# Performance work log

Hardware: AMD Instinct MI355X
Metric: run time of the kernel (lower is better)

The kernel has to match this reference:

```python
import math
import jax, jax.numpy as jnp
import numpy as np

B, N, E, H, DPOS = 64, 196, 768, 16, 3
DH = E // H


def rel_pos(num_patches):
    # deterministic relative-position encodings [N, N, 3] = (dx, dy, d^2)
    v = int(math.isqrt(num_patches))
    ind = jnp.arange(v)[None, :] - jnp.arange(v)[:, None]          # [v, v]
    indx = jnp.tile(ind, (v, v))                                    # [N, N]
    indy = jnp.repeat(jnp.repeat(ind, v, axis=0), v, axis=1)       # [N, N]
    indd = indx ** 2 + indy ** 2
    return jnp.stack([indx, indy, indd], axis=-1).astype(jnp.float32)


def setup_inputs() -> dict:
    key = jax.random.key(0)
    ks = jax.random.split(key, 9)
    std = 0.02  # trunc_normal std used by the module's init
    return {
        "q": jax.random.normal(ks[0], (B, N, E), jnp.float32),
        "k": jax.random.normal(ks[1], (B, N, E), jnp.float32),
        "v": jax.random.normal(ks[2], (B, N, E), jnp.float32),
        "mask": jnp.ones((B, 1, N, N), jnp.bool_),
        "Wq": jax.random.normal(ks[3], (E, E), jnp.float32) * std,
        "Wk": jax.random.normal(ks[4], (E, E), jnp.float32) * std,
        "Wv": jax.random.normal(ks[5], (E, E), jnp.float32) * std,
        "Wo": jax.random.normal(ks[6], (E, E), jnp.float32) * std,
        "bo": jnp.zeros((E,), jnp.float32),
        "Wpos": jax.random.normal(ks[7], (H, DPOS), jnp.float32) * std,
        "bpos": jnp.zeros((H,), jnp.float32),
        "gating": jnp.ones((H,), jnp.float32),
    }


def reference(q, k, v, mask, Wq, Wk, Wv, Wo, bo, Wpos, bpos, gating):
    b, n, _ = q.shape

    def heads(x, W):  # [b, n, E] -> [b, H, n, DH]
        return (x @ W.T).reshape(b, n, H, DH).transpose(0, 2, 1, 3)

    Q, K, V = heads(q, Wq), heads(k, Wk), heads(v, Wv)

    energy = jnp.einsum('bhqd,bhkd->bhqk', Q, K) / math.sqrt(DH)
    energy = jnp.where(mask, energy, -jnp.inf)
    content = jax.nn.softmax(energy, axis=-1)                      # [b, H, n, n]

    rel = rel_pos(n)                                               # [n, n, 3]
    pos = jnp.einsum('qkp,hp->hqk', rel, Wpos) + bpos[:, None, None]
    pos = jax.nn.softmax(pos, axis=-1)[None]                       # [1, H, n, n]

    g = jax.nn.sigmoid(gating)[None, :, None, None]
    score = (1.0 - g) * content + g * pos
    score = score / jnp.sum(score, axis=-1, keepdims=True)

    attn = jnp.einsum('bhqk,bhkd->bhqd', score, V)
    out = attn.transpose(0, 2, 1, 3).reshape(b, n, E) @ Wo.T + bo
    return out
```

## Files before the change

kernel.cpp:

```cpp
#include <hip/hip_runtime.h>
#include <hip/hip_bf16.h>

#define BB 64
#define NN 196
#define EE 768
#define HH 16
#define DHH 48

typedef short bf16x8 __attribute__((ext_vector_type(8)));
typedef float f32x4 __attribute__((ext_vector_type(4)));
typedef unsigned short u16;
typedef unsigned short u16x8 __attribute__((ext_vector_type(8)));
typedef unsigned int u32;

static __device__ __forceinline__ u16 f2bf(float f) {
  union { float f; u32 u; } un; un.f = f;
  u32 u = un.u;
  u32 r = (u + 0x7fffu + ((u >> 16) & 1u)) >> 16;
  return (u16)r;
}

static __device__ __forceinline__ u16 f2bf_hw(float f) {
  __hip_bfloat16 h = __float2bfloat16(f);
  return __builtin_bit_cast(u16, h);
}

#define GLOAD16(GP, LP)                                                        \
  __builtin_amdgcn_global_load_lds(                                            \
      (const __attribute__((address_space(1))) void*)(GP),                     \
      (__attribute__((address_space(3))) void*)(LP), 16, 0, 0)

static __device__ __forceinline__ int xcd_swz(int bid, int nwg) {
  int q = nwg >> 3, r = nwg & 7;
  int xcd = bid & 7, i = bid >> 3;
  return (xcd < r ? xcd * (q + 1) : r * (q + 1) + (xcd - r) * q) + i;
}

__global__ __launch_bounds__(64) void pos_kernel(const float* __restrict__ Wpos,
                                                 const float* __restrict__ bpos,
                                                 float* __restrict__ pos) {
  int bid = blockIdx.x;
  int h = bid / NN, q = bid % NN;
  int lane = threadIdx.x;
  float w0 = Wpos[h * 3 + 0], w1 = Wpos[h * 3 + 1], w2 = Wpos[h * 3 + 2];
  float bb = bpos[h];
  int qx = q % 14, qy = q / 14;
  float e[4];
  float mx = -1e30f;
#pragma unroll
  for (int i = 0; i < 4; ++i) {
    int k = lane + 64 * i;
    float val = -1e30f;
    if (k < NN) {
      int kx = k % 14, ky = k / 14;
      float dx = (float)(kx - qx), dy = (float)(ky - qy);
      val = w0 * dx + w1 * dy + w2 * (dx * dx + dy * dy) + bb;
    }
    e[i] = val;
    mx = fmaxf(mx, val);
  }
#pragma unroll
  for (int off = 1; off < 64; off <<= 1) mx = fmaxf(mx, __shfl_xor(mx, off));
  float s = 0.f;
#pragma unroll
  for (int i = 0; i < 4; ++i) {
    int k = lane + 64 * i;
    float p = (k < NN) ? expf(e[i] - mx) : 0.f;
    e[i] = p;
    s += p;
  }
#pragma unroll
  for (int off = 1; off < 64; off <<= 1) s += __shfl_xor(s, off);
  float inv = 1.f / s;
#pragma unroll
  for (int i = 0; i < 4; ++i) {
    int k = lane + 64 * i;
    if (k < NN) pos[(size_t)h * NN * NN + (size_t)q * NN + k] = e[i] * inv;
  }
}

__global__ __launch_bounds__(256) void cvtw_kernel(const float* __restrict__ W0,
                                                   const float* __restrict__ W1,
                                                   const float* __restrict__ W2,
                                                   const float* __restrict__ W3,
                                                   u16* __restrict__ out) {
  const float* Ws[4] = {W0, W1, W2, W3};
  int mat = blockIdx.y;
  const float* src = Ws[mat];
  int idx = blockIdx.x * 256 + threadIdx.x;
  float4 f = ((const float4*)src)[idx];
  short4 s;
  s.x = (short)f2bf_hw(f.x);
  s.y = (short)f2bf_hw(f.y);
  s.z = (short)f2bf_hw(f.z);
  s.w = (short)f2bf_hw(f.w);
  *(short4*)(out + (size_t)mat * EE * EE + (size_t)idx * 4) = s;
}

template <bool A_F32, bool OUT_F32>
static __device__ __forceinline__ void gemm_body(const void* __restrict__ Aptr,
                                                 const u16* __restrict__ Wb,
                                                 void* __restrict__ Yptr,
                                                 const float* __restrict__ bias,
                                                 int m0, int n0) {
  constexpr int ABYTES = A_F32 ? (128 * 32 * 4) : (128 * 32 * 2);
  __shared__ unsigned char Asb[2][ABYTES];
  __shared__ u16 Bs[2][128 * 32];
  const int tid = threadIdx.x;
  const int lane = tid & 63, wid = tid >> 6;
  const int wm = wid >> 1, wn = wid & 1;
  const int r16 = lane & 15, g4 = lane >> 4;
  f32x4 acc[4][4];
#pragma unroll
  for (int i = 0; i < 4; ++i)
#pragma unroll
    for (int j = 0; j < 4; ++j) acc[i][j] = (f32x4){0.f, 0.f, 0.f, 0.f};

  auto stage = [&](int buf, int k0) {
#pragma unroll
    for (int c = 0; c < 2; ++c) {
      int s = c * 256 + tid;
      GLOAD16(Wb + (size_t)(n0 + (s >> 2)) * EE + k0 + (s & 3) * 8,
              (u16*)&Bs[buf][0] + s * 8);
    }
    if (A_F32) {
#pragma unroll
      for (int c = 0; c < 4; ++c) {
        int s = c * 256 + tid;
        int row = s >> 3;
        int cf = ((s & 7) ^ (row & 7)) * 4;
        GLOAD16((const float*)Aptr + (size_t)(m0 + row) * EE + k0 + cf,
                &Asb[buf][0] + s * 16);
      }
    } else {
#pragma unroll
      for (int c = 0; c < 2; ++c) {
        int s = c * 256 + tid;
        GLOAD16((const u16*)Aptr + (size_t)(m0 + (s >> 2)) * EE + k0 + (s & 3) * 8,
                &Asb[buf][0] + s * 16);
      }
    }
  };

  stage(0, 0);
  __syncthreads();
  int buf = 0;
  for (int t = 0; t < 24; ++t) {
    if (t < 23) stage(buf ^ 1, (t + 1) * 32);
    bf16x8 af[4], bfr[4];
#pragma unroll
    for (int i = 0; i < 4; ++i) {
      int r = wm * 64 + i * 16 + r16;
      if (A_F32) {
        const char* rowp = (const char*)&Asb[buf][0] + r * 128;
        int lo = (g4 * 32) ^ ((r & 7) << 4);
        f32x4 l4 = *(const f32x4*)(rowp + lo);
        f32x4 h4 = *(const f32x4*)(rowp + (lo ^ 16));
        u16x8 fr;
        fr[0] = f2bf_hw(l4[0]); fr[1] = f2bf_hw(l4[1]);
        fr[2] = f2bf_hw(l4[2]); fr[3] = f2bf_hw(l4[3]);
        fr[4] = f2bf_hw(h4[0]); fr[5] = f2bf_hw(h4[1]);
        fr[6] = f2bf_hw(h4[2]); fr[7] = f2bf_hw(h4[3]);
        af[i] = __builtin_bit_cast(bf16x8, fr);
      } else {
        af[i] = *(const bf16x8*)((const u16*)&Asb[buf][0] + r * 32 + g4 * 8);
      }
    }
#pragma unroll
    for (int j = 0; j < 4; ++j)
      bfr[j] = *(const bf16x8*)&Bs[buf][(wn * 64 + j * 16 + r16) * 32 + g4 * 8];
#pragma unroll
    for (int i = 0; i < 4; ++i)
#pragma unroll
      for (int j = 0; j < 4; ++j)
        acc[i][j] = __builtin_amdgcn_mfma_f32_16x16x32_bf16(af[i], bfr[j], acc[i][j], 0, 0, 0);
    __syncthreads();
    buf ^= 1;
  }
#pragma unroll
  for (int i = 0; i < 4; ++i) {
    int row = m0 + wm * 64 + i * 16 + g4 * 4;
#pragma unroll
    for (int j = 0; j < 4; ++j) {
      int col = n0 + wn * 64 + j * 16 + r16;
#pragma unroll
      for (int v = 0; v < 4; ++v) {
        float val = acc[i][j][v];
        if (OUT_F32)
          ((float*)Yptr)[(size_t)(row + v) * EE + col] = val + bias[col];
        else
          ((u16*)Yptr)[(size_t)(row + v) * EE + col] = f2bf(val);
      }
    }
  }
}

__global__ __launch_bounds__(256) void qkv_gemm(const float* __restrict__ q,
                                                const float* __restrict__ k,
                                                const float* __restrict__ v,
                                                const u16* __restrict__ Wqb,
                                                const u16* __restrict__ Wkb,
                                                const u16* __restrict__ Wvb,
                                                u16* __restrict__ Qp,
                                                u16* __restrict__ Kp,
                                                u16* __restrict__ Vp) {
  int sid = xcd_swz(blockIdx.x, 3 * 98 * 6);
  int z = sid / 588, rem = sid % 588;
  int m0 = (rem / 6) * 128, n0 = (rem % 6) * 128;
  const float* A = (z == 0) ? q : (z == 1) ? k : v;
  const u16* W = (z == 0) ? Wqb : (z == 1) ? Wkb : Wvb;
  u16* Y = (z == 0) ? Qp : (z == 1) ? Kp : Vp;
  gemm_body<true, false>(A, W, Y, nullptr, m0, n0);
}

__global__ __launch_bounds__(256) void out_gemm(const u16* __restrict__ ctx,
                                                const u16* __restrict__ Wob,
                                                float* __restrict__ out,
                                                const float* __restrict__ bo) {
  int sid = xcd_swz(blockIdx.x, 98 * 6);
  int m0 = (sid / 6) * 128, n0 = (sid % 6) * 128;
  gemm_body<false, true>(ctx, Wob, out, bo, m0, n0);
}

__global__ __launch_bounds__(512) void attn_kernel(const u16* __restrict__ Qp,
                                                   const u16* __restrict__ Kp,
                                                   const u16* __restrict__ Vp,
                                                   const float* __restrict__ pos,
                                                   const float* __restrict__ gating,
                                                   u16* __restrict__ ctx) {
  __shared__ u16 Qs[208 * 72];
  __shared__ u16 Ks[208 * 72];
  __shared__ u16 Vt[48 * 232];
  __shared__ u16 sc[8][16 * 232];
  int bh = blockIdx.x;
  int b = bh >> 4, h = bh & 15;
  int tid = threadIdx.x;
  {
    u32* z = (u32*)&Qs[0];
    for (int i = tid; i < (208 * 72) / 2; i += 512) z[i] = 0u;
    z = (u32*)&Ks[0];
    for (int i = tid; i < (208 * 72) / 2; i += 512) z[i] = 0u;
    z = (u32*)&Vt[0];
    for (int i = tid; i < (48 * 232) / 2; i += 512) z[i] = 0u;
  }
  __syncthreads();
  const u16* Qb = Qp + (size_t)b * NN * EE + h * DHH;
  const u16* Kb = Kp + (size_t)b * NN * EE + h * DHH;
  const u16* Vb = Vp + (size_t)b * NN * EE + h * DHH;
  for (int c = tid; c < NN * 12; c += 512) {
    int row = c / 12, k4 = (c % 12) * 4;
    short4 v = *(const short4*)(Qb + (size_t)row * EE + k4);
    *(short4*)&Qs[row * 72 + k4] = v;
  }
  for (int c = tid; c < NN * 12; c += 512) {
    int row = c / 12, k4 = (c % 12) * 4;
    short4 v = *(const short4*)(Kb + (size_t)row * EE + k4);
    *(short4*)&Ks[row * 72 + k4] = v;
  }
  for (int c = tid; c < NN * 12; c += 512) {
    int key = c / 12, d4 = (c % 12) * 4;
    short4 v = *(const short4*)(Vb + (size_t)key * EE + d4);
    Vt[(d4 + 0) * 232 + key] = (u16)v.x;
    Vt[(d4 + 1) * 232 + key] = (u16)v.y;
    Vt[(d4 + 2) * 232 + key] = (u16)v.z;
    Vt[(d4 + 3) * 232 + key] = (u16)v.w;
  }
  __syncthreads();

  int wid = tid >> 6, lane = tid & 63;
  int r16 = lane & 15, g4 = lane >> 4;
  float g = 1.f / (1.f + expf(-gating[h]));
  float omg = 1.f - g;
  u16* scw = &sc[wid][0];
  const float scale = 0.14433756729740643f;
  const float* posh = pos + (size_t)h * NN * NN;

  for (int rt = wid; rt < 13; rt += 8) {
    int q0 = rt * 16;
    bf16x8 aQ0 = *(const bf16x8*)&Qs[(q0 + r16) * 72 + g4 * 8];
    bf16x8 aQ1 = *(const bf16x8*)&Qs[(q0 + r16) * 72 + 32 + g4 * 8];
    f32x4 e[13];
#pragma unroll
    for (int ct = 0; ct < 13; ++ct) {
      bf16x8 b0 = *(const bf16x8*)&Ks[(ct * 16 + r16) * 72 + g4 * 8];
      bf16x8 b1 = *(const bf16x8*)&Ks[(ct * 16 + r16) * 72 + 32 + g4 * 8];
      f32x4 t = (f32x4){0.f, 0.f, 0.f, 0.f};
      t = __builtin_amdgcn_mfma_f32_16x16x32_bf16(aQ0, b0, t, 0, 0, 0);
      t = __builtin_amdgcn_mfma_f32_16x16x32_bf16(aQ1, b1, t, 0, 0, 0);
      e[ct] = t;
    }
    float mx[4] = {-1e30f, -1e30f, -1e30f, -1e30f};
#pragma unroll
    for (int ct = 0; ct < 13; ++ct) {
      int cix = ct * 16 + r16;
      bool valid = cix < NN;
#pragma unroll
      for (int v = 0; v < 4; ++v) {
        float ev = e[ct][v] * scale;
        ev = valid ? ev : -1e30f;
        e[ct][v] = ev;
        mx[v] = fmaxf(mx[v], ev);
      }
    }
#pragma unroll
    for (int v = 0; v < 4; ++v)
#pragma unroll
      for (int off = 1; off < 16; off <<= 1) mx[v] = fmaxf(mx[v], __shfl_xor(mx[v], off));
    float sm[4] = {0.f, 0.f, 0.f, 0.f};
#pragma unroll
    for (int ct = 0; ct < 13; ++ct)
#pragma unroll
      for (int v = 0; v < 4; ++v) {
        float p = __expf(e[ct][v] - mx[v]);
        e[ct][v] = p;
        sm[v] += p;
      }
#pragma unroll
    for (int v = 0; v < 4; ++v)
#pragma unroll
      for (int off = 1; off < 16; off <<= 1) sm[v] += __shfl_xor(sm[v], off);
    float inv[4];
#pragma unroll
    for (int v = 0; v < 4; ++v) inv[v] = 1.f / sm[v];
    int qg[4];
#pragma unroll
    for (int v = 0; v < 4; ++v) qg[v] = q0 + g4 * 4 + v;
    float t2[4] = {0.f, 0.f, 0.f, 0.f};
#pragma unroll
    for (int ct = 0; ct < 13; ++ct) {
      int cix = ct * 16 + r16;
      bool valid = cix < NN;
#pragma unroll
      for (int v = 0; v < 4; ++v) {
        float content = e[ct][v] * inv[v];
        float pv = 0.f;
        if (valid && qg[v] < NN) pv = posh[(size_t)qg[v] * NN + cix];
        float s = omg * content + g * pv;
        e[ct][v] = s;
        t2[v] += s;
      }
    }
#pragma unroll
    for (int v = 0; v < 4; ++v)
#pragma unroll
      for (int off = 1; off < 16; off <<= 1) t2[v] += __shfl_xor(t2[v], off);
    float inv2[4];
#pragma unroll
    for (int v = 0; v < 4; ++v) inv2[v] = 1.f / t2[v];
#pragma unroll
    for (int ct = 0; ct < 14; ++ct)
#pragma unroll
      for (int v = 0; v < 4; ++v) {
        float s = (ct < 13) ? e[ct][v] * inv2[v] : 0.f;
        scw[(g4 * 4 + v) * 232 + ct * 16 + r16] = f2bf(s);
      }
    asm volatile("s_waitcnt lgkmcnt(0)" ::: "memory");
#pragma unroll
    for (int dt = 0; dt < 3; ++dt) {
      f32x4 pv = (f32x4){0.f, 0.f, 0.f, 0.f};
#pragma unroll
      for (int kt = 0; kt < 7; ++kt) {
        bf16x8 aS = *(const bf16x8*)&scw[r16 * 232 + kt * 32 + g4 * 8];
        bf16x8 bV = *(const bf16x8*)&Vt[(dt * 16 + r16) * 232 + kt * 32 + g4 * 8];
        pv = __builtin_amdgcn_mfma_f32_16x16x32_bf16(aS, bV, pv, 0, 0, 0);
      }
#pragma unroll
      for (int v = 0; v < 4; ++v) {
        if (qg[v] < NN)
          ctx[((size_t)b * NN + qg[v]) * EE + h * DHH + dt * 16 + r16] = f2bf(pv[v]);
      }
    }
  }
}

extern "C" void kernel_launch(void* const* d_in, const int* in_sizes, int n_in,
                              void* d_out, int out_size, void* d_ws, size_t ws_size,
                              hipStream_t stream) {
  const float* q = (const float*)d_in[0];
  const float* k = (const float*)d_in[1];
  const float* v = (const float*)d_in[2];
  const float* Wq = (const float*)d_in[4];
  const float* Wk = (const float*)d_in[5];
  const float* Wv = (const float*)d_in[6];
  const float* Wo = (const float*)d_in[7];
  const float* bo = (const float*)d_in[8];
  const float* Wpos = (const float*)d_in[9];
  const float* bpos = (const float*)d_in[10];
  const float* gating = (const float*)d_in[11];
  float* out = (float*)d_out;

  char* ws = (char*)d_ws;
  const size_t elems = (size_t)BB * NN * EE;
  u16* Qp = (u16*)ws;
  u16* Kp = Qp + elems;
  u16* Vp = Kp + elems;
  u16* ctx = Vp + elems;
  float* pos = (float*)(ws + 4 * elems * sizeof(u16));
  u16* Wqb = (u16*)(ws + 4 * elems * sizeof(u16) + (size_t)HH * NN * NN * sizeof(float));
  u16* Wkb = Wqb + (size_t)EE * EE;
  u16* Wvb = Wkb + (size_t)EE * EE;
  u16* Wob = Wvb + (size_t)EE * EE;

  hipLaunchKernelGGL(pos_kernel, dim3(HH * NN), dim3(64), 0, stream, Wpos, bpos, pos);
  hipLaunchKernelGGL(cvtw_kernel, dim3(EE * EE / 4 / 256, 4), dim3(256), 0, stream,
                     Wq, Wk, Wv, Wo, Wqb);

  hipLaunchKernelGGL(qkv_gemm, dim3(3 * 98 * 6), dim3(256), 0, stream,
                     q, k, v, Wqb, Wkb, Wvb, Qp, Kp, Vp);

  hipLaunchKernelGGL(attn_kernel, dim3(BB * HH), dim3(512), 0, stream,
                     Qp, Kp, Vp, pos, gating, ctx);

  hipLaunchKernelGGL(out_gemm, dim3(98 * 6), dim3(256), 0, stream,
                     ctx, Wob, out, bo);
}
```

Baseline: 200.5 us.

## Widen GEMM tiles to 128x256 and convert fp32 A to bf16 once per stage

The QKV and output GEMMs now use 128x256 tiles, so each wave computes 64x128 and the block count halves (882 and 294 blocks). The fp32 activation tile is now loaded into registers, converted to bf16 once and written to shared memory after the MFMA loop. Before, fp32 was staged in LDS and converted on every fragment read. This cuts LDS footprint and repeated conversion work and reuses A across more columns, but doubles accumulator registers (launch bounds 256,2) and gives fewer blocks to fill the CUs.

```diff
diff --git a/kernel.cpp b/kernel.cpp
--- a/kernel.cpp
+++ b/kernel.cpp
@@ -103,77 +103,81 @@
                                                  void* __restrict__ Yptr,
                                                  const float* __restrict__ bias,
                                                  int m0, int n0) {
-  constexpr int ABYTES = A_F32 ? (128 * 32 * 4) : (128 * 32 * 2);
-  __shared__ unsigned char Asb[2][ABYTES];
-  __shared__ u16 Bs[2][128 * 32];
+  __shared__ u16 As[2][128 * 32];
+  __shared__ u16 Bs[2][256 * 32];
   const int tid = threadIdx.x;
   const int lane = tid & 63, wid = tid >> 6;
   const int wm = wid >> 1, wn = wid & 1;
   const int r16 = lane & 15, g4 = lane >> 4;
-  f32x4 acc[4][4];
+  f32x4 acc[4][8];
 #pragma unroll
   for (int i = 0; i < 4; ++i)
 #pragma unroll
-    for (int j = 0; j < 4; ++j) acc[i][j] = (f32x4){0.f, 0.f, 0.f, 0.f};
-
-  auto stage = [&](int buf, int k0) {
+    for (int j = 0; j < 8; ++j) acc[i][j] = (f32x4){0.f, 0.f, 0.f, 0.f};
+
+  float4 fa[4];
+  const int arow0 = tid >> 2, aseg = tid & 3;
+
+  auto loadA = [&](int k0) {
 #pragma unroll
     for (int c = 0; c < 2; ++c) {
+      const float* p =
+          (const float*)Aptr + (size_t)(m0 + c * 64 + arow0) * EE + k0 + aseg * 8;
+      fa[c * 2 + 0] = ((const float4*)p)[0];
+      fa[c * 2 + 1] = ((const float4*)p)[1];
+    }
+  };
+  auto writeA = [&](int buf) {
+#pragma unroll
+    for (int c = 0; c < 2; ++c) {
+      u16x8 s0;
+      s0[0] = f2bf_hw(fa[c * 2].x);     s0[1] = f2bf_hw(fa[c * 2].y);
+      s0[2] = f2bf_hw(fa[c * 2].z);     s0[3] = f2bf_hw(fa[c * 2].w);
+      s0[4] = f2bf_hw(fa[c * 2 + 1].x); s0[5] = f2bf_hw(fa[c * 2 + 1].y);
+      s0[6] = f2bf_hw(fa[c * 2 + 1].z); s0[7] = f2bf_hw(fa[c * 2 + 1].w);
+      *(u16x8*)&As[buf][(c * 256 + tid) * 8] = s0;
+    }
+  };
+  auto stageA16 = [&](int buf, int k0) {
+#pragma unroll
+    for (int c = 0; c < 2; ++c) {
+      const u16* p =
+          (const u16*)Aptr + (size_t)(m0 + c * 64 + arow0) * EE + k0 + aseg * 8;
+      GLOAD16(p, &As[buf][(c * 256 + tid) * 8]);
+    }
+  };
+  auto stageB = [&](int buf, int k0) {
+#pragma unroll
+    for (int c = 0; c < 4; ++c) {
       int s = c * 256 + tid;
       GLOAD16(Wb + (size_t)(n0 + (s >> 2)) * EE + k0 + (s & 3) * 8,
-              (u16*)&Bs[buf][0] + s * 8);
-    }
-    if (A_F32) {
-#pragma unroll
-      for (int c = 0; c < 4; ++c) {
-        int s = c * 256 + tid;
-        int row = s >> 3;
-        int cf = ((s & 7) ^ (row & 7)) * 4;
-        GLOAD16((const float*)Aptr + (size_t)(m0 + row) * EE + k0 + cf,
-                &Asb[buf][0] + s * 16);
-      }
-    } else {
-#pragma unroll
-      for (int c = 0; c < 2; ++c) {
-        int s = c * 256 + tid;
-        GLOAD16((const u16*)Aptr + (size_t)(m0 + (s >> 2)) * EE + k0 + (s & 3) * 8,
-                &Asb[buf][0] + s * 16);
-      }
+              &Bs[buf][s * 8]);
     }
   };
 
-  stage(0, 0);
+  if (A_F32) { loadA(0); stageB(0, 0); writeA(0); }
+  else       { stageA16(0, 0); stageB(0, 0); }
   __syncthreads();
   int buf = 0;
   for (int t = 0; t < 24; ++t) {
-    if (t < 23) stage(buf ^ 1, (t + 1) * 32);
-    bf16x8 af[4], bfr[4];
-#pragma unroll
-    for (int i = 0; i < 4; ++i) {
-      int r = wm * 64 + i * 16 + r16;
-      if (A_F32) {
-        const char* rowp = (const char*)&Asb[buf][0] + r * 128;
-        int lo = (g4 * 32) ^ ((r & 7) << 4);
-        f32x4 l4 = *(const f32x4*)(rowp + lo);
-        f32x4 h4 = *(const f32x4*)(rowp + (lo ^ 16));
-        u16x8 fr;
-        fr[0] = f2bf_hw(l4[0]); fr[1] = f2bf_hw(l4[1]);
-        fr[2] = f2bf_hw(l4[2]); fr[3] = f2bf_hw(l4[3]);
-        fr[4] = f2bf_hw(h4[0]); fr[5] = f2bf_hw(h4[1]);
-        fr[6] = f2bf_hw(h4[2]); fr[7] = f2bf_hw(h4[3]);
-        af[i] = __builtin_bit_cast(bf16x8, fr);
-      } else {
-        af[i] = *(const bf16x8*)((const u16*)&Asb[buf][0] + r * 32 + g4 * 8);
-      }
-    }
-#pragma unroll
-    for (int j = 0; j < 4; ++j)
-      bfr[j] = *(const bf16x8*)&Bs[buf][(wn * 64 + j * 16 + r16) * 32 + g4 * 8];
+    if (t < 23) {
+      if (A_F32) loadA((t + 1) * 32);
+      else       stageA16(buf ^ 1, (t + 1) * 32);
+      stageB(buf ^ 1, (t + 1) * 32);
+    }
+    bf16x8 af[4], bfr[8];
 #pragma unroll
     for (int i = 0; i < 4; ++i)
-#pragma unroll
-      for (int j = 0; j < 4; ++j)
+      af[i] = *(const bf16x8*)&As[buf][(wm * 64 + i * 16 + r16) * 32 + g4 * 8];
+#pragma unroll
+    for (int j = 0; j < 8; ++j)
+      bfr[j] = *(const bf16x8*)&Bs[buf][(wn * 128 + j * 16 + r16) * 32 + g4 * 8];
+#pragma unroll
+    for (int i = 0; i < 4; ++i)
+#pragma unroll
+      for (int j = 0; j < 8; ++j)
         acc[i][j] = __builtin_amdgcn_mfma_f32_16x16x32_bf16(af[i], bfr[j], acc[i][j], 0, 0, 0);
+    if (A_F32 && t < 23) writeA(buf ^ 1);
     __syncthreads();
     buf ^= 1;
   }
@@ -181,8 +185,8 @@
   for (int i = 0; i < 4; ++i) {
     int row = m0 + wm * 64 + i * 16 + g4 * 4;
 #pragma unroll
-    for (int j = 0; j < 4; ++j) {
-      int col = n0 + wn * 64 + j * 16 + r16;
+    for (int j = 0; j < 8; ++j) {
+      int col = n0 + wn * 128 + j * 16 + r16;
 #pragma unroll
       for (int v = 0; v < 4; ++v) {
         float val = acc[i][j][v];
@@ -195,30 +199,30 @@
   }
 }
 
-__global__ __launch_bounds__(256) void qkv_gemm(const float* __restrict__ q,
-                                                const float* __restrict__ k,
-                                                const float* __restrict__ v,
-                                                const u16* __restrict__ Wqb,
-                                                const u16* __restrict__ Wkb,
-                                                const u16* __restrict__ Wvb,
-                                                u16* __restrict__ Qp,
-                                                u16* __restrict__ Kp,
-                                                u16* __restrict__ Vp) {
-  int sid = xcd_swz(blockIdx.x, 3 * 98 * 6);
-  int z = sid / 588, rem = sid % 588;
-  int m0 = (rem / 6) * 128, n0 = (rem % 6) * 128;
+__global__ __launch_bounds__(256, 2) void qkv_gemm(const float* __restrict__ q,
+                                                   const float* __restrict__ k,
+                                                   const float* __restrict__ v,
+                                                   const u16* __restrict__ Wqb,
+                                                   const u16* __restrict__ Wkb,
+                                                   const u16* __restrict__ Wvb,
+                                                   u16* __restrict__ Qp,
+                                                   u16* __restrict__ Kp,
+                                                   u16* __restrict__ Vp) {
+  int sid = xcd_swz(blockIdx.x, 3 * 98 * 3);
+  int z = sid / 294, rem = sid % 294;
+  int m0 = (rem / 3) * 128, n0 = (rem % 3) * 256;
   const float* A = (z == 0) ? q : (z == 1) ? k : v;
   const u16* W = (z == 0) ? Wqb : (z == 1) ? Wkb : Wvb;
   u16* Y = (z == 0) ? Qp : (z == 1) ? Kp : Vp;
   gemm_body<true, false>(A, W, Y, nullptr, m0, n0);
 }
 
-__global__ __launch_bounds__(256) void out_gemm(const u16* __restrict__ ctx,
-                                                const u16* __restrict__ Wob,
-                                                float* __restrict__ out,
-                                                const float* __restrict__ bo) {
-  int sid = xcd_swz(blockIdx.x, 98 * 6);
-  int m0 = (sid / 6) * 128, n0 = (sid % 6) * 128;
+__global__ __launch_bounds__(256, 2) void out_gemm(const u16* __restrict__ ctx,
+                                                   const u16* __restrict__ Wob,
+                                                   float* __restrict__ out,
+                                                   const float* __restrict__ bo) {
+  int sid = xcd_swz(blockIdx.x, 98 * 3);
+  int m0 = (sid / 3) * 128, n0 = (sid % 3) * 256;
   gemm_body<false, true>(ctx, Wob, out, bo, m0, n0);
 }
 
@@ -405,12 +409,12 @@
   hipLaunchKernelGGL(cvtw_kernel, dim3(EE * EE / 4 / 256, 4), dim3(256), 0, stream,
                      Wq, Wk, Wv, Wo, Wqb);
 
-  hipLaunchKernelGGL(qkv_gemm, dim3(3 * 98 * 6), dim3(256), 0, stream,
+  hipLaunchKernelGGL(qkv_gemm, dim3(3 * 98 * 3), dim3(256), 0, stream,
                      q, k, v, Wqb, Wkb, Wvb, Qp, Kp, Vp);
 
   hipLaunchKernelGGL(attn_kernel, dim3(BB * HH), dim3(512), 0, stream,
                      Qp, Kp, Vp, pos, gating, ctx);
 
-  hipLaunchKernelGGL(out_gemm, dim3(98 * 6), dim3(256), 0, stream,
+  hipLaunchKernelGGL(out_gemm, dim3(98 * 3), dim3(256), 0, stream,
                      ctx, Wob, out, bo);
 }
```

After: 213.1 us. +6.3%, slower.
